# Optimization experiments

Measured on AMD Instinct MI355X. Metric: run time of the kernel, lower is better.

The kernel has to match this reference:

```python
import jax, jax.numpy as jnp
import numpy as np

N_EXPERTS = 8
D_MODEL = 512
HIDDEN = 1408
TOTAL_TOKENS = 32768  # 4096 tokens per expert, equal contiguous segments


def setup_inputs() -> dict:
    key = jax.random.key(0)
    k1, k2, k3 = jax.random.split(key, 3)
    sorted_x = jax.random.normal(k1, (TOTAL_TOKENS, D_MODEL), dtype=jnp.float32)
    # weights init: normal(std=0.02) as in the torch module
    w12 = 0.02 * jax.random.normal(k2, (N_EXPERTS, 2 * HIDDEN, D_MODEL), dtype=jnp.float32)
    w3 = 0.02 * jax.random.normal(k3, (N_EXPERTS, D_MODEL, HIDDEN), dtype=jnp.float32)
    tpe = TOTAL_TOKENS // N_EXPERTS
    expert_starts = jnp.arange(N_EXPERTS, dtype=jnp.int32) * tpe
    expert_ends = expert_starts + tpe
    return {"sorted_x": sorted_x, "w12": w12, "w3": w3,
            "expert_starts": expert_starts, "expert_ends": expert_ends}


def reference(sorted_x, w12, w3, expert_starts, expert_ends):
    """Grouped SwiGLU expert MLP over tokens pre-sorted by expert.

    setup_inputs() produces equal-sized contiguous expert segments, so each
    expert processes tpe = T // E tokens (fixed-size grouped GEMM).
    """
    E, twoH, D = w12.shape
    T = sorted_x.shape[0]
    tpe = T // E  # tokens per expert segment

    # gather each expert's contiguous token block: (E, tpe, D)
    x_e = jax.vmap(lambda s: jax.lax.dynamic_slice(sorted_x, (s, 0), (tpe, D)))(expert_starts)

    # grouped GEMM 1 (fused gate+up): (E, tpe, 2H)
    h12 = jnp.einsum('etd,ehd->eth', x_e, w12).astype(jnp.float32)
    h1, h2 = jnp.split(h12, 2, axis=-1)
    h = jax.nn.silu(h1) * h2  # SwiGLU

    # grouped GEMM 2 (down-proj): (E, tpe, D)
    out = jnp.einsum('eth,edh->etd', h.astype(sorted_x.dtype), w3).astype(jnp.float32)
    # segments are contiguous and in expert order -> concat == reshape
    return out.reshape(T, D)
```

## Files before the change

kernel.cpp:

```cpp
#include <hip/hip_runtime.h>
#include <stdint.h>

#define TPE 4096
#define DM 512
#define HID 1408
#define NE 8

#define N4X   4194304
#define N4W12 2883584
#define N4W3  1441792

typedef unsigned short u16;
typedef __attribute__((ext_vector_type(8))) __bf16 bf16x8;
typedef __attribute__((ext_vector_type(4))) float f32x4;

__device__ __forceinline__ u16 f2bf(float f) {
  union { float f; uint32_t u; } v; v.f = f;
  uint32_t u = v.u;
  u += 0x7fffu + ((u >> 16) & 1u);
  return (u16)(u >> 16);
}

__global__ void cvt_xw12(const float* __restrict__ x, const float* __restrict__ w12,
                         u16* __restrict__ xb, u16* __restrict__ w12b) {
  int i = blockIdx.x * blockDim.x + threadIdx.x;
  const float* src; u16* dst; int off;
  if (i < N4X) { src = x;   dst = xb;   off = i; }
  else         { src = w12; dst = w12b; off = i - N4X; }
  float4 v = reinterpret_cast<const float4*>(src)[off];
  union { u16 s[4]; uint2 u2; } o;
  o.s[0] = f2bf(v.x); o.s[1] = f2bf(v.y); o.s[2] = f2bf(v.z); o.s[3] = f2bf(v.w);
  reinterpret_cast<uint2*>(dst)[off] = o.u2;
}

template <int ROWS>
__device__ __forceinline__ void stage_tile64(u16* lds, const u16* g, int lda,
                                             int wave, int lane) {
  const int srow = lane >> 3;
  const int gchunk = (lane & 7) ^ srow;
#pragma unroll
  for (int r = 0; r < ROWS / 32; ++r) {
    const int row0 = (wave * (ROWS / 32) + r) * 8;
    const u16* gp = g + (size_t)(row0 + srow) * lda + gchunk * 8;
    u16* lp = lds + row0 * 64;
    __builtin_amdgcn_global_load_lds((const __attribute__((address_space(1))) void*)gp,
                                     (__attribute__((address_space(3))) void*)lp,
                                     16, 0, 0);
  }
}

__device__ __forceinline__ bf16x8 read_frag(const u16* lds, int row, int kchunk) {
  return *reinterpret_cast<const bf16x8*>(&lds[row * 64 + (((kchunk ^ (row & 7)) << 3))]);
}

__global__ __launch_bounds__(256, 2)
void gemm1_swiglu(const u16* __restrict__ xb, const u16* __restrict__ w12b,
                  u16* __restrict__ hb, const float* __restrict__ w3f,
                  u16* __restrict__ w3b) {
  __shared__ u16 sA[128 * 64];
  __shared__ u16 sBg[128 * 64];
  __shared__ u16 sBu[128 * 64];
  const int e = blockIdx.x;
  const int y = blockIdx.y;
  const int tid = threadIdx.x;

  if (y >= 352) {
    const int c = e + 8 * (y - 352);
    const float4* src = reinterpret_cast<const float4*>(w3f) + (size_t)c * 4096;
    uint2* dst = reinterpret_cast<uint2*>(w3b) + (size_t)c * 4096;
#pragma unroll
    for (int it = 0; it < 16; ++it) {
      float4 v = src[it * 256 + tid];
      union { u16 s[4]; uint2 u2; } o;
      o.s[0] = f2bf(v.x); o.s[1] = f2bf(v.y); o.s[2] = f2bf(v.z); o.s[3] = f2bf(v.w);
      dst[it * 256 + tid] = o.u2;
    }
    return;
  }

  const int mt = y / 11, nt = y % 11;
  const int wave = tid >> 6, lane = tid & 63;
  const int wm = wave >> 1, wn = wave & 1;
  const int quad = lane >> 4, rr = lane & 15;

  const u16* A  = xb + (size_t)(e * TPE + mt * 128) * DM;
  const u16* Bg = w12b + (size_t)e * (2 * HID) * DM + (size_t)(nt * 128) * DM;
  const u16* Bu = Bg + (size_t)HID * DM;

  f32x4 zero = {0.f, 0.f, 0.f, 0.f};
  f32x4 accg[4][4], accu[4][4];
#pragma unroll
  for (int i = 0; i < 4; ++i)
#pragma unroll
    for (int j = 0; j < 4; ++j) { accg[i][j] = zero; accu[i][j] = zero; }

  for (int k0 = 0; k0 < DM; k0 += 64) {
    stage_tile64<128>(sA, A + k0, DM, wave, lane);
    stage_tile64<128>(sBg, Bg + k0, DM, wave, lane);
    stage_tile64<128>(sBu, Bu + k0, DM, wave, lane);
    __syncthreads();

#pragma unroll
    for (int kk = 0; kk < 2; ++kk) {
      const int kc = kk * 4 + quad;
      bf16x8 af[4], bg[4], bu[4];
#pragma unroll
      for (int mi = 0; mi < 4; ++mi)
        af[mi] = read_frag(sA, wm * 64 + mi * 16 + rr, kc);
#pragma unroll
      for (int ni = 0; ni < 4; ++ni) {
        bg[ni] = read_frag(sBg, wn * 64 + ni * 16 + rr, kc);
        bu[ni] = read_frag(sBu, wn * 64 + ni * 16 + rr, kc);
      }
#pragma unroll
      for (int mi = 0; mi < 4; ++mi)
#pragma unroll
        for (int ni = 0; ni < 4; ++ni) {
          accg[mi][ni] = __builtin_amdgcn_mfma_f32_16x16x32_bf16(af[mi], bg[ni], accg[mi][ni], 0, 0, 0);
          accu[mi][ni] = __builtin_amdgcn_mfma_f32_16x16x32_bf16(af[mi], bu[ni], accu[mi][ni], 0, 0, 0);
        }
    }
    __syncthreads();
  }

  const size_t rowbase = (size_t)(e * TPE + mt * 128 + wm * 64);
  const int colbase = nt * 128 + wn * 64;
#pragma unroll
  for (int mi = 0; mi < 4; ++mi)
#pragma unroll
    for (int ni = 0; ni < 4; ++ni)
#pragma unroll
      for (int r2 = 0; r2 < 4; ++r2) {
        float g = accg[mi][ni][r2];
        float u = accu[mi][ni][r2];
        float s = (g / (1.f + __expf(-g))) * u;
        size_t row = rowbase + mi * 16 + quad * 4 + r2;
        int col = colbase + ni * 16 + rr;
        hb[row * HID + col] = f2bf(s);
      }
}

__global__ __launch_bounds__(256, 2)
void gemm2(const u16* __restrict__ hb, const u16* __restrict__ w3b,
           float* __restrict__ out) {
  __shared__ u16 sA[128 * 64];
  __shared__ u16 sB[256 * 64];
  const int e = blockIdx.x;
  const int mt = blockIdx.y >> 1, nt = blockIdx.y & 1;
  const int tid = threadIdx.x, wave = tid >> 6, lane = tid & 63;
  const int wm = wave >> 1, wn = wave & 1;
  const int quad = lane >> 4, rr = lane & 15;

  const u16* A = hb + (size_t)(e * TPE + mt * 128) * HID;
  const u16* B = w3b + (size_t)e * DM * HID + (size_t)(nt * 256) * HID;

  f32x4 zero = {0.f, 0.f, 0.f, 0.f};
  f32x4 acc[4][8];
#pragma unroll
  for (int i = 0; i < 4; ++i)
#pragma unroll
    for (int j = 0; j < 8; ++j) acc[i][j] = zero;

  for (int k0 = 0; k0 < HID; k0 += 64) {
    stage_tile64<128>(sA, A + k0, HID, wave, lane);
    stage_tile64<256>(sB, B + k0, HID, wave, lane);
    __syncthreads();

#pragma unroll
    for (int kk = 0; kk < 2; ++kk) {
      const int kc = kk * 4 + quad;
      bf16x8 af[4], bfr[8];
#pragma unroll
      for (int mi = 0; mi < 4; ++mi)
        af[mi] = read_frag(sA, wm * 64 + mi * 16 + rr, kc);
#pragma unroll
      for (int ni = 0; ni < 8; ++ni)
        bfr[ni] = read_frag(sB, wn * 128 + ni * 16 + rr, kc);
#pragma unroll
      for (int mi = 0; mi < 4; ++mi)
#pragma unroll
        for (int ni = 0; ni < 8; ++ni)
          acc[mi][ni] = __builtin_amdgcn_mfma_f32_16x16x32_bf16(af[mi], bfr[ni], acc[mi][ni], 0, 0, 0);
    }
    __syncthreads();
  }

  const size_t rowbase = (size_t)(e * TPE + mt * 128 + wm * 64);
  const int colbase = nt * 256 + wn * 128;
#pragma unroll
  for (int mi = 0; mi < 4; ++mi)
#pragma unroll
    for (int ni = 0; ni < 8; ++ni)
#pragma unroll
      for (int r2 = 0; r2 < 4; ++r2) {
        size_t row = rowbase + mi * 16 + quad * 4 + r2;
        int col = colbase + ni * 16 + rr;
        out[row * DM + col] = acc[mi][ni][r2];
      }
}

extern "C" void kernel_launch(void* const* d_in, const int* in_sizes, int n_in,
                              void* d_out, int out_size, void* d_ws, size_t ws_size,
                              hipStream_t stream) {
  (void)in_sizes; (void)n_in; (void)out_size; (void)ws_size;
  const float* x   = (const float*)d_in[0];
  const float* w12 = (const float*)d_in[1];
  const float* w3  = (const float*)d_in[2];
  float* out = (float*)d_out;

  char* ws = (char*)d_ws;
  u16* xb   = (u16*)(ws);
  u16* w12b = (u16*)(ws + (size_t)33554432);
  u16* w3b  = (u16*)(ws + (size_t)33554432 + 23068672);
  u16* hb   = (u16*)(ws + (size_t)33554432 + 23068672 + 11534336);

  const int n4 = N4X + N4W12;
  cvt_xw12<<<n4 / 256, 256, 0, stream>>>(x, w12, xb, w12b);

  gemm1_swiglu<<<dim3(8, 352 + 44), 256, 0, stream>>>(xb, w12b, hb, w3, w3b);
  gemm2<<<dim3(8, 64), 256, 0, stream>>>(hb, w3b, out);
}
```

Baseline: 304.9 us.

## Restructure gemm1 into 256x128 tiles with double-buffered LDS and interleaved MFMA phases

The fused gate/up GEMM now uses 512-thread blocks computing 256-row by 128-column (gate+up) tiles, with double-buffered LDS stages loaded asynchronously while the current stage is consumed. The inner loop is split into four MFMA phases separated by barriers and s_setprio bumps, interleaving next-stage global->LDS loads with compute. This raises data reuse per block and aims to hide load latency behind MFMA work, at the cost of 128KB LDS per block, which limits occupancy, plus extra barriers. The w3 conversion blocks are resized to match the new block size.

```diff
diff --git a/kernel.cpp b/kernel.cpp
--- a/kernel.cpp
+++ b/kernel.cpp
@@ -8,7 +8,6 @@
 
 #define N4X   4194304
 #define N4W12 2883584
-#define N4W3  1441792
 
 typedef unsigned short u16;
 typedef __attribute__((ext_vector_type(8))) __bf16 bf16x8;
@@ -49,86 +48,170 @@
   }
 }
 
+__device__ __forceinline__ void stage256(u16* lds, const u16* g, int lda,
+                                         int wave, int lane) {
+  const int srow = lane >> 3;
+  const int gchunk = (lane & 7) ^ srow;
+#pragma unroll
+  for (int r = 0; r < 4; ++r) {
+    const int row0 = (r * 8 + wave) * 8;
+    const u16* gp = g + (size_t)(row0 + srow) * lda + gchunk * 8;
+    u16* lp = lds + row0 * 64;
+    __builtin_amdgcn_global_load_lds((const __attribute__((address_space(1))) void*)gp,
+                                     (__attribute__((address_space(3))) void*)lp,
+                                     16, 0, 0);
+  }
+}
+
+__device__ __forceinline__ void stageB256(u16* lds, const u16* Bg, const u16* Bu,
+                                          int wave, int lane) {
+  const int srow = lane >> 3;
+  const int gchunk = (lane & 7) ^ srow;
+#pragma unroll
+  for (int r = 0; r < 4; ++r) {
+    const int rowblk = r * 8 + wave;
+    const int row0 = rowblk * 8;
+    const u16* base = (rowblk < 16) ? (Bg + (size_t)row0 * DM)
+                                    : (Bu + (size_t)(row0 - 128) * DM);
+    const u16* gp = base + (size_t)srow * DM + gchunk * 8;
+    u16* lp = lds + row0 * 64;
+    __builtin_amdgcn_global_load_lds((const __attribute__((address_space(1))) void*)gp,
+                                     (__attribute__((address_space(3))) void*)lp,
+                                     16, 0, 0);
+  }
+}
+
 __device__ __forceinline__ bf16x8 read_frag(const u16* lds, int row, int kchunk) {
   return *reinterpret_cast<const bf16x8*>(&lds[row * 64 + (((kchunk ^ (row & 7)) << 3))]);
 }
 
-__global__ __launch_bounds__(256, 2)
+__global__ __launch_bounds__(512, 2)
 void gemm1_swiglu(const u16* __restrict__ xb, const u16* __restrict__ w12b,
                   u16* __restrict__ hb, const float* __restrict__ w3f,
                   u16* __restrict__ w3b) {
-  __shared__ u16 sA[128 * 64];
-  __shared__ u16 sBg[128 * 64];
-  __shared__ u16 sBu[128 * 64];
+  __shared__ u16 sA[2][256 * 64];
+  __shared__ u16 sB[2][256 * 64];
   const int e = blockIdx.x;
   const int y = blockIdx.y;
   const int tid = threadIdx.x;
 
-  if (y >= 352) {
-    const int c = e + 8 * (y - 352);
+  if (y >= 176) {
+    const int c = e + 8 * (y - 176);
     const float4* src = reinterpret_cast<const float4*>(w3f) + (size_t)c * 4096;
     uint2* dst = reinterpret_cast<uint2*>(w3b) + (size_t)c * 4096;
 #pragma unroll
-    for (int it = 0; it < 16; ++it) {
-      float4 v = src[it * 256 + tid];
+    for (int it = 0; it < 8; ++it) {
+      float4 v = src[it * 512 + tid];
       union { u16 s[4]; uint2 u2; } o;
       o.s[0] = f2bf(v.x); o.s[1] = f2bf(v.y); o.s[2] = f2bf(v.z); o.s[3] = f2bf(v.w);
-      dst[it * 256 + tid] = o.u2;
+      dst[it * 512 + tid] = o.u2;
     }
     return;
   }
 
   const int mt = y / 11, nt = y % 11;
   const int wave = tid >> 6, lane = tid & 63;
-  const int wm = wave >> 1, wn = wave & 1;
+  const int wm = wave >> 2, wn = wave & 3;
   const int quad = lane >> 4, rr = lane & 15;
 
-  const u16* A  = xb + (size_t)(e * TPE + mt * 128) * DM;
+  const u16* A  = xb + (size_t)(e * TPE + mt * 256) * DM;
   const u16* Bg = w12b + (size_t)e * (2 * HID) * DM + (size_t)(nt * 128) * DM;
   const u16* Bu = Bg + (size_t)HID * DM;
 
   f32x4 zero = {0.f, 0.f, 0.f, 0.f};
-  f32x4 accg[4][4], accu[4][4];
-#pragma unroll
-  for (int i = 0; i < 4; ++i)
-#pragma unroll
-    for (int j = 0; j < 4; ++j) { accg[i][j] = zero; accu[i][j] = zero; }
-
-  for (int k0 = 0; k0 < DM; k0 += 64) {
-    stage_tile64<128>(sA, A + k0, DM, wave, lane);
-    stage_tile64<128>(sBg, Bg + k0, DM, wave, lane);
-    stage_tile64<128>(sBu, Bu + k0, DM, wave, lane);
+  f32x4 accg[8][2], accu[8][2];
+#pragma unroll
+  for (int i = 0; i < 8; ++i)
+#pragma unroll
+    for (int j = 0; j < 2; ++j) { accg[i][j] = zero; accu[i][j] = zero; }
+
+  stage256(sA[0], A, DM, wave, lane);
+  stageB256(sB[0], Bg, Bu, wave, lane);
+  __syncthreads();
+
+#pragma unroll 2
+  for (int t = 0; t < 8; ++t) {
+    const int cur = t & 1, nxt = cur ^ 1;
+    const u16* cA = sA[cur];
+    const u16* cB = sB[cur];
+    bf16x8 af[4][2], bg[2][2], bu[2][2];
+
+    if (t < 7) stage256(sA[nxt], A + (t + 1) * 64, DM, wave, lane);
+#pragma unroll
+    for (int mi = 0; mi < 4; ++mi)
+#pragma unroll
+      for (int kk = 0; kk < 2; ++kk)
+        af[mi][kk] = read_frag(cA, wm * 128 + mi * 16 + rr, kk * 4 + quad);
+#pragma unroll
+    for (int ni = 0; ni < 2; ++ni)
+#pragma unroll
+      for (int kk = 0; kk < 2; ++kk)
+        bg[ni][kk] = read_frag(cB, wn * 32 + ni * 16 + rr, kk * 4 + quad);
+    __builtin_amdgcn_s_barrier();
+    __builtin_amdgcn_s_setprio(1);
+#pragma unroll
+    for (int mi = 0; mi < 4; ++mi)
+#pragma unroll
+      for (int ni = 0; ni < 2; ++ni)
+#pragma unroll
+        for (int kk = 0; kk < 2; ++kk)
+          accg[mi][ni] = __builtin_amdgcn_mfma_f32_16x16x32_bf16(af[mi][kk], bg[ni][kk], accg[mi][ni], 0, 0, 0);
+    __builtin_amdgcn_s_setprio(0);
+    __builtin_amdgcn_s_barrier();
+
+    if (t < 7) stageB256(sB[nxt], Bg + (t + 1) * 64, Bu + (t + 1) * 64, wave, lane);
+#pragma unroll
+    for (int ni = 0; ni < 2; ++ni)
+#pragma unroll
+      for (int kk = 0; kk < 2; ++kk)
+        bu[ni][kk] = read_frag(cB, 128 + wn * 32 + ni * 16 + rr, kk * 4 + quad);
+    __builtin_amdgcn_s_barrier();
+    __builtin_amdgcn_s_setprio(1);
+#pragma unroll
+    for (int mi = 0; mi < 4; ++mi)
+#pragma unroll
+      for (int ni = 0; ni < 2; ++ni)
+#pragma unroll
+        for (int kk = 0; kk < 2; ++kk)
+          accu[mi][ni] = __builtin_amdgcn_mfma_f32_16x16x32_bf16(af[mi][kk], bu[ni][kk], accu[mi][ni], 0, 0, 0);
+    __builtin_amdgcn_s_setprio(0);
+    __builtin_amdgcn_s_barrier();
+
+#pragma unroll
+    for (int mi = 0; mi < 4; ++mi)
+#pragma unroll
+      for (int kk = 0; kk < 2; ++kk)
+        af[mi][kk] = read_frag(cA, wm * 128 + 64 + mi * 16 + rr, kk * 4 + quad);
+    __builtin_amdgcn_s_barrier();
+    __builtin_amdgcn_s_setprio(1);
+#pragma unroll
+    for (int mi = 0; mi < 4; ++mi)
+#pragma unroll
+      for (int ni = 0; ni < 2; ++ni)
+#pragma unroll
+        for (int kk = 0; kk < 2; ++kk)
+          accg[4 + mi][ni] = __builtin_amdgcn_mfma_f32_16x16x32_bf16(af[mi][kk], bg[ni][kk], accg[4 + mi][ni], 0, 0, 0);
+    __builtin_amdgcn_s_setprio(0);
+    __builtin_amdgcn_s_barrier();
+
+    __builtin_amdgcn_s_setprio(1);
+#pragma unroll
+    for (int mi = 0; mi < 4; ++mi)
+#pragma unroll
+      for (int ni = 0; ni < 2; ++ni)
+#pragma unroll
+        for (int kk = 0; kk < 2; ++kk)
+          accu[4 + mi][ni] = __builtin_amdgcn_mfma_f32_16x16x32_bf16(af[mi][kk], bu[ni][kk], accu[4 + mi][ni], 0, 0, 0);
+    __builtin_amdgcn_s_setprio(0);
     __syncthreads();
-
-#pragma unroll
-    for (int kk = 0; kk < 2; ++kk) {
-      const int kc = kk * 4 + quad;
-      bf16x8 af[4], bg[4], bu[4];
-#pragma unroll
-      for (int mi = 0; mi < 4; ++mi)
-        af[mi] = read_frag(sA, wm * 64 + mi * 16 + rr, kc);
-#pragma unroll
-      for (int ni = 0; ni < 4; ++ni) {
-        bg[ni] = read_frag(sBg, wn * 64 + ni * 16 + rr, kc);
-        bu[ni] = read_frag(sBu, wn * 64 + ni * 16 + rr, kc);
-      }
-#pragma unroll
-      for (int mi = 0; mi < 4; ++mi)
-#pragma unroll
-        for (int ni = 0; ni < 4; ++ni) {
-          accg[mi][ni] = __builtin_amdgcn_mfma_f32_16x16x32_bf16(af[mi], bg[ni], accg[mi][ni], 0, 0, 0);
-          accu[mi][ni] = __builtin_amdgcn_mfma_f32_16x16x32_bf16(af[mi], bu[ni], accu[mi][ni], 0, 0, 0);
-        }
-    }
-    __syncthreads();
-  }
-
-  const size_t rowbase = (size_t)(e * TPE + mt * 128 + wm * 64);
-  const int colbase = nt * 128 + wn * 64;
-#pragma unroll
-  for (int mi = 0; mi < 4; ++mi)
-#pragma unroll
-    for (int ni = 0; ni < 4; ++ni)
+  }
+
+  const size_t rowbase = (size_t)(e * TPE + mt * 256 + wm * 128);
+  const int colbase = nt * 128 + wn * 32;
+#pragma unroll
+  for (int mi = 0; mi < 8; ++mi)
+#pragma unroll
+    for (int ni = 0; ni < 2; ++ni)
 #pragma unroll
       for (int r2 = 0; r2 < 4; ++r2) {
         float g = accg[mi][ni][r2];
@@ -217,6 +300,6 @@
   const int n4 = N4X + N4W12;
   cvt_xw12<<<n4 / 256, 256, 0, stream>>>(x, w12, xb, w12b);
 
-  gemm1_swiglu<<<dim3(8, 352 + 44), 256, 0, stream>>>(xb, w12b, hb, w3, w3b);
+  gemm1_swiglu<<<dim3(8, 176 + 44), 512, 0, stream>>>(xb, w12b, hb, w3, w3b);
   gemm2<<<dim3(8, 64), 256, 0, stream>>>(hb, w3b, out);
 }
```

Result: slower. 320.8 us (+5.2%).

## Move w3 conversion into grid-stride cvt kernel and shrink gemm2 tiles

Applied to the files above, without the earlier changes.

The w3 fp32-to-bf16 conversion moves out of extra blocks in the gemm1 grid and into a single grid-stride conversion kernel that handles x, w12 and w3 with a fixed 2048-block grid. gemm2's output tile drops from 128x256 to 128x128, doubling its grid to 1024 blocks, and its launch bound rises to 3 blocks per SM. The smaller tiles aim for more parallelism and occupancy in gemm2, which previously had only 512 blocks. In exchange, each gemm2 block does less MFMA work per byte loaded, and each A tile of hb is fetched from global memory twice as often.

```diff
diff --git a/kernel.cpp b/kernel.cpp
--- a/kernel.cpp
+++ b/kernel.cpp
@@ -21,16 +21,23 @@
   return (u16)(u >> 16);
 }
 
-__global__ void cvt_xw12(const float* __restrict__ x, const float* __restrict__ w12,
-                         u16* __restrict__ xb, u16* __restrict__ w12b) {
-  int i = blockIdx.x * blockDim.x + threadIdx.x;
-  const float* src; u16* dst; int off;
-  if (i < N4X) { src = x;   dst = xb;   off = i; }
-  else         { src = w12; dst = w12b; off = i - N4X; }
+__device__ __forceinline__ void cvt4(const float* __restrict__ src,
+                                     u16* __restrict__ dst, int off) {
   float4 v = reinterpret_cast<const float4*>(src)[off];
   union { u16 s[4]; uint2 u2; } o;
   o.s[0] = f2bf(v.x); o.s[1] = f2bf(v.y); o.s[2] = f2bf(v.z); o.s[3] = f2bf(v.w);
   reinterpret_cast<uint2*>(dst)[off] = o.u2;
+}
+
+__global__ void cvt_all(const float* __restrict__ x, const float* __restrict__ w12,
+                        const float* __restrict__ w3,
+                        u16* __restrict__ xb, u16* __restrict__ w12b,
+                        u16* __restrict__ w3b) {
+  const int stride = gridDim.x * blockDim.x;
+  const int i0 = blockIdx.x * blockDim.x + threadIdx.x;
+  for (int j = i0; j < N4X; j += stride)   cvt4(x, xb, j);
+  for (int j = i0; j < N4W12; j += stride) cvt4(w12, w12b, j);
+  for (int j = i0; j < N4W3; j += stride)  cvt4(w3, w3b, j);
 }
 
 template <int ROWS>
@@ -55,28 +62,13 @@
 
 __global__ __launch_bounds__(256, 2)
 void gemm1_swiglu(const u16* __restrict__ xb, const u16* __restrict__ w12b,
-                  u16* __restrict__ hb, const float* __restrict__ w3f,
-                  u16* __restrict__ w3b) {
+                  u16* __restrict__ hb) {
   __shared__ u16 sA[128 * 64];
   __shared__ u16 sBg[128 * 64];
   __shared__ u16 sBu[128 * 64];
   const int e = blockIdx.x;
   const int y = blockIdx.y;
   const int tid = threadIdx.x;
-
-  if (y >= 352) {
-    const int c = e + 8 * (y - 352);
-    const float4* src = reinterpret_cast<const float4*>(w3f) + (size_t)c * 4096;
-    uint2* dst = reinterpret_cast<uint2*>(w3b) + (size_t)c * 4096;
-#pragma unroll
-    for (int it = 0; it < 16; ++it) {
-      float4 v = src[it * 256 + tid];
-      union { u16 s[4]; uint2 u2; } o;
-      o.s[0] = f2bf(v.x); o.s[1] = f2bf(v.y); o.s[2] = f2bf(v.z); o.s[3] = f2bf(v.w);
-      dst[it * 256 + tid] = o.u2;
-    }
-    return;
-  }
 
   const int mt = y / 11, nt = y % 11;
   const int wave = tid >> 6, lane = tid & 63;
@@ -140,57 +132,57 @@
       }
 }
 
-__global__ __launch_bounds__(256, 2)
+__global__ __launch_bounds__(256, 3)
 void gemm2(const u16* __restrict__ hb, const u16* __restrict__ w3b,
            float* __restrict__ out) {
   __shared__ u16 sA[128 * 64];
-  __shared__ u16 sB[256 * 64];
+  __shared__ u16 sB[128 * 64];
   const int e = blockIdx.x;
-  const int mt = blockIdx.y >> 1, nt = blockIdx.y & 1;
+  const int mt = blockIdx.y >> 2, nt = blockIdx.y & 3;
   const int tid = threadIdx.x, wave = tid >> 6, lane = tid & 63;
   const int wm = wave >> 1, wn = wave & 1;
   const int quad = lane >> 4, rr = lane & 15;
 
   const u16* A = hb + (size_t)(e * TPE + mt * 128) * HID;
-  const u16* B = w3b + (size_t)e * DM * HID + (size_t)(nt * 256) * HID;
+  const u16* B = w3b + (size_t)e * DM * HID + (size_t)(nt * 128) * HID;
 
   f32x4 zero = {0.f, 0.f, 0.f, 0.f};
-  f32x4 acc[4][8];
+  f32x4 acc[4][4];
 #pragma unroll
   for (int i = 0; i < 4; ++i)
 #pragma unroll
-    for (int j = 0; j < 8; ++j) acc[i][j] = zero;
+    for (int j = 0; j < 4; ++j) acc[i][j] = zero;
 
   for (int k0 = 0; k0 < HID; k0 += 64) {
     stage_tile64<128>(sA, A + k0, HID, wave, lane);
-    stage_tile64<256>(sB, B + k0, HID, wave, lane);
+    stage_tile64<128>(sB, B + k0, HID, wave, lane);
     __syncthreads();
 
 #pragma unroll
     for (int kk = 0; kk < 2; ++kk) {
       const int kc = kk * 4 + quad;
-      bf16x8 af[4], bfr[8];
+      bf16x8 af[4], bfr[4];
 #pragma unroll
       for (int mi = 0; mi < 4; ++mi)
         af[mi] = read_frag(sA, wm * 64 + mi * 16 + rr, kc);
 #pragma unroll
-      for (int ni = 0; ni < 8; ++ni)
-        bfr[ni] = read_frag(sB, wn * 128 + ni * 16 + rr, kc);
-#pragma unroll
-      for (int mi = 0; mi < 4; ++mi)
-#pragma unroll
-        for (int ni = 0; ni < 8; ++ni)
+      for (int ni = 0; ni < 4; ++ni)
+        bfr[ni] = read_frag(sB, wn * 64 + ni * 16 + rr, kc);
+#pragma unroll
+      for (int mi = 0; mi < 4; ++mi)
+#pragma unroll
+        for (int ni = 0; ni < 4; ++ni)
           acc[mi][ni] = __builtin_amdgcn_mfma_f32_16x16x32_bf16(af[mi], bfr[ni], acc[mi][ni], 0, 0, 0);
     }
     __syncthreads();
   }
 
   const size_t rowbase = (size_t)(e * TPE + mt * 128 + wm * 64);
-  const int colbase = nt * 256 + wn * 128;
+  const int colbase = nt * 128 + wn * 64;
 #pragma unroll
   for (int mi = 0; mi < 4; ++mi)
 #pragma unroll
-    for (int ni = 0; ni < 8; ++ni)
+    for (int ni = 0; ni < 4; ++ni)
 #pragma unroll
       for (int r2 = 0; r2 < 4; ++r2) {
         size_t row = rowbase + mi * 16 + quad * 4 + r2;
@@ -214,9 +206,7 @@
   u16* w3b  = (u16*)(ws + (size_t)33554432 + 23068672);
   u16* hb   = (u16*)(ws + (size_t)33554432 + 23068672 + 11534336);
 
-  const int n4 = N4X + N4W12;
-  cvt_xw12<<<n4 / 256, 256, 0, stream>>>(x, w12, xb, w12b);
-
-  gemm1_swiglu<<<dim3(8, 352 + 44), 256, 0, stream>>>(xb, w12b, hb, w3, w3b);
-  gemm2<<<dim3(8, 64), 256, 0, stream>>>(hb, w3b, out);
-}
+  cvt_all<<<2048, 256, 0, stream>>>(x, w12, w3, xb, w12b, w3b);
+  gemm1_swiglu<<<dim3(8, 352), 256, 0, stream>>>(xb, w12b, hb);
+  gemm2<<<dim3(8, 128), 256, 0, stream>>>(hb, w3b, out);
+}
```

After: 331.5 us. +8.7%, slower.
